# Performance work log

Measured on AMD Instinct MI355X. Metric: run time of the kernel, lower is better.

The kernel has to match this reference:

```python
import jax, jax.numpy as jnp
import numpy as np

B, H, W, DIM = 2, 128, 128, 256
NB, EXP, HEADS = 16, 8, 8
BS = DIM // NB          # AFNO block size = 16
DH = DIM // HEADS       # head dim = 32
EPS = 1e-5
LAM = 0.01              # softshrink threshold


def _ln(x, g, b):
    mu = jnp.mean(x, axis=-1, keepdims=True)
    var = jnp.mean((x - mu) ** 2, axis=-1, keepdims=True)
    return (x - mu) * jax.lax.rsqrt(var + EPS) * g + b


def _afno(x, w1, b1, w2, b2):
    # FourCastNet AFNO2D: block-diagonal complex MLP in Fourier space
    bias = x
    Bx, Hx, Wx, C = x.shape
    xf = jnp.fft.rfft2(x, axes=(1, 2), norm='ortho')          # [B,H,W//2+1,C] complex
    xf = xf.reshape(Bx, Hx, Wx // 2 + 1, NB, BS)
    xr, xi = jnp.real(xf), jnp.imag(xf)
    mm = lambda t, w: jnp.einsum('bhwni,nio->bhwno', t, w)
    o1r = jax.nn.relu(mm(xr, w1[0]) - mm(xi, w1[1]) + b1[0])
    o1i = jax.nn.relu(mm(xi, w1[0]) + mm(xr, w1[1]) + b1[1])
    o2r = mm(o1r, w2[0]) - mm(o1i, w2[1]) + b2[0]
    o2i = mm(o1i, w2[0]) + mm(o1r, w2[1]) + b2[1]
    shrink = lambda t: jnp.sign(t) * jnp.maximum(jnp.abs(t) - LAM, 0.0)
    xf = (shrink(o2r) + 1j * shrink(o2i)).reshape(Bx, Hx, Wx // 2 + 1, C)
    out = jnp.fft.irfft2(xf, s=(Hx, Wx), axes=(1, 2), norm='ortho')
    return out + bias


def _galerkin(h, wq, bq, wk, bk, wv, bv, lnk_g, lnk_b, lnv_g, lnv_b, wo, bo):
    # softmax-free linear attention: Q (LN(K)^T LN(V)) / N
    Bx, N, C = h.shape
    split = lambda t, w, b: (t @ w.T + b).reshape(Bx, N, HEADS, DH).transpose(0, 2, 1, 3)
    q = split(h, wq, bq)
    k = split(h, wk, bk)
    v = split(h, wv, bv)
    k = _ln(k, lnk_g[None, :, None, :], lnk_b[None, :, None, :])
    v = _ln(v, lnv_g[None, :, None, :], lnv_b[None, :, None, :])
    kv = jnp.einsum('bhnd,bhne->bhde', k, v) / N     # [B,h,dh,dh]
    out = jnp.einsum('bhnd,bhde->bhne', q, kv)       # [B,h,N,dh]
    out = out.transpose(0, 2, 1, 3).reshape(Bx, N, C)
    return out @ wo.T + bo


def _forward(x, afno_w1, afno_b1, afno_w2, afno_b2,
             wq, bq, wk, bk, wv, bv, lnk_g, lnk_b, lnv_g, lnv_b, wo, bo,
             w_up, b_up, w_down, b_down,
             n1_g, n1_b, n2_g, n2_b, n3_g, n3_b):
    Bx, Hx, Wx, C = x.shape
    # 1) AFNO spectral mixing block
    x = x + _afno(_ln(x, n1_g, n1_b), afno_w1, afno_b1, afno_w2, afno_b2)
    # 2) Galerkin linear attention block
    x = _ln(x, n2_g, n2_b)
    h = x.reshape(Bx, Hx * Wx, C)
    x = x + _galerkin(h, wq, bq, wk, bk, wv, bv,
                      lnk_g, lnk_b, lnv_g, lnv_b, wo, bo).reshape(Bx, Hx, Wx, C)
    # 3) pointwise-conv (1x1) FFN block; conv1x1 over BCHW == per-token linear in BHWC
    x = _ln(x, n3_g, n3_b)
    h = jax.nn.gelu(x @ w_up.T + b_up, approximate=False)
    x = x + h @ w_down.T + b_down
    return x


def setup_inputs() -> dict:
    key = jax.random.key(0)
    ks = jax.random.split(key, 24)
    r = lambda i, shape, s: jax.random.normal(ks[i], shape, dtype=jnp.float32) * s
    z = lambda shape: jnp.zeros(shape, dtype=jnp.float32)
    o = lambda shape: jnp.ones(shape, dtype=jnp.float32)
    return dict(
        x=r(0, (B, H, W, DIM), 1.0),
        afno_w1=r(1, (2, NB, BS, BS * EXP), 0.02),
        afno_b1=r(2, (2, NB, BS * EXP), 0.02),
        afno_w2=r(3, (2, NB, BS * EXP, BS), 0.02),
        afno_b2=r(4, (2, NB, BS), 0.02),
        wq=r(5, (DIM, DIM), 0.02), bq=z((DIM,)),
        wk=r(6, (DIM, DIM), 0.02), bk=z((DIM,)),
        wv=r(7, (DIM, DIM), 0.02), bv=z((DIM,)),
        lnk_g=o((HEADS, DH)), lnk_b=z((HEADS, DH)),
        lnv_g=o((HEADS, DH)), lnv_b=z((HEADS, DH)),
        wo=r(8, (DIM, DIM), 0.02), bo=z((DIM,)),
        w_up=r(9, (DIM * EXP, DIM), 0.02), b_up=z((DIM * EXP,)),
        w_down=r(10, (DIM, DIM * EXP), 0.02), b_down=z((DIM,)),
        n1_g=o((DIM,)), n1_b=z((DIM,)),
        n2_g=o((DIM,)), n2_b=z((DIM,)),
        n3_g=o((DIM,)), n3_b=z((DIM,)),
    )


def reference(x, afno_w1, afno_b1, afno_w2, afno_b2,
              wq, bq, wk, bk, wv, bv, lnk_g, lnk_b, lnv_g, lnv_b, wo, bo,
              w_up, b_up, w_down, b_down,
              n1_g, n1_b, n2_g, n2_b, n3_g, n3_b):
    return _forward(x, afno_w1, afno_b1, afno_w2, afno_b2,
                    wq, bq, wk, bk, wv, bv, lnk_g, lnk_b, lnv_g, lnv_b, wo, bo,
                    w_up, b_up, w_down, b_down,
                    n1_g, n1_b, n2_g, n2_b, n3_g, n3_b)
```

## Files before the change

### kernel.cpp

```cpp
#include <hip/hip_runtime.h>


typedef unsigned short u16;
typedef unsigned int u32;
typedef __attribute__((ext_vector_type(8))) short bf16x8;
typedef __attribute__((ext_vector_type(8))) unsigned short u16x8;
typedef __attribute__((ext_vector_type(4))) float f32x4;
#define DEV __device__ __forceinline__

constexpr int Cch = 256;
constexpr float EPSN = 1e-5f, LAM = 0.01f;
constexpr float TWO_PI = 6.283185307179586f;

DEV float b2f(u16 u) { return __uint_as_float(((u32)u) << 16); }
DEV u16 f2b(float f) {
  u32 x = __float_as_uint(f);
  return (u16)((x + 0x7FFFu + ((x >> 16) & 1u)) >> 16);
}

DEV void put2(u16* tw, int m, int idx, float v) {
  u16 hi = f2b(v);
  tw[m * 16384 + idx] = hi;
  tw[(m + 1) * 16384 + idx] = f2b(v - b2f(hi));
}

__global__ __launch_bounds__(128) void k_twid(u16* __restrict__ tw) {
  int p = blockIdx.x, q = threadIdx.x;
  int idx = p * 128 + q;
  float ang = TWO_PI * (float)((p * q) & 127) * (1.0f / 128.0f);
  float c = cosf(ang), s = sinf(ang);
  put2(tw, 0, idx, c * (1.0f / 128.0f));
  put2(tw, 2, idx, s * (1.0f / 128.0f));
  put2(tw, 4, idx, -s * (1.0f / 128.0f));
  put2(tw, 6, idx, c);
  put2(tw, 8, idx, s);
  put2(tw, 10, idx, -s);
  u16* wmh = tw + 196608;
  u16* wml = tw + 217088;
  for (int k = q; k < 160; k += 128) {
    float v = 0.0f;
    if (k < 65) {
      float sc = (k == 0 || k == 64) ? 1.0f : 2.0f;
      v = sc * cosf(TWO_PI * (float)((p * k) & 127) * (1.0f / 128.0f)) * (1.0f / 128.0f);
    } else if (k < 130) {
      int kk = k - 65;
      float sc = (kk == 0 || kk == 64) ? 1.0f : 2.0f;
      v = -sc * sinf(TWO_PI * (float)((p * kk) & 127) * (1.0f / 128.0f)) * (1.0f / 128.0f);
    }
    u16 hi = f2b(v);
    wmh[p * 160 + k] = hi;
    wml[p * 160 + k] = f2b(v - b2f(hi));
  }
}

__global__ __launch_bounds__(256) void k_wpack(const float* __restrict__ w1,
                                               const float* __restrict__ w2,
                                               u16* __restrict__ W1h, u16* __restrict__ W1l,
                                               u16* __restrict__ W2h, u16* __restrict__ W2l) {
  int idx = blockIdx.x * 256 + threadIdx.x;
  if (idx < 131072) {
    int n = idx >> 13, rem = idx & 8191;
    int out = rem >> 5, k = rem & 31;
    float v;
    if (out < 128)
      v = (k < 16) ? w1[((size_t)n * 16 + k) * 128 + out]
                   : -w1[((size_t)(16 + n) * 16 + (k - 16)) * 128 + out];
    else {
      int o = out - 128;
      v = (k < 16) ? w1[((size_t)(16 + n) * 16 + k) * 128 + o]
                   : w1[((size_t)n * 16 + (k - 16)) * 128 + o];
    }
    u16 hi = f2b(v);
    W1h[idx] = hi; W1l[idx] = f2b(v - b2f(hi));
  } else if (idx < 262144) {
    int id2 = idx - 131072;
    int n = id2 >> 13, rem = id2 & 8191;
    int out2 = rem >> 8, k = rem & 255;
    float v;
    if (out2 < 16)
      v = (k < 128) ? w2[((size_t)n * 128 + k) * 16 + out2]
                    : -w2[((size_t)(16 + n) * 128 + (k - 128)) * 16 + out2];
    else {
      int o = out2 - 16;
      v = (k < 128) ? w2[((size_t)(16 + n) * 128 + k) * 16 + o]
                    : w2[((size_t)n * 128 + (k - 128)) * 16 + o];
    }
    u16 hi = f2b(v);
    W2h[id2] = hi; W2l[id2] = f2b(v - b2f(hi));
  }
}

__global__ __launch_bounds__(256) void k_cvt2(const float* __restrict__ s0,
                                              const float* __restrict__ s1,
                                              u16* __restrict__ d0,
                                              u16* __restrict__ d1, int n) {
  int i = blockIdx.x * 256 + threadIdx.x;
  if (i < n) { d0[i] = f2b(s0[i]); d1[i] = f2b(s1[i]); }
}

template<int INF>
__global__ __launch_bounds__(256) void k_ln(const void* __restrict__ in,
                                            const float* __restrict__ g,
                                            const float* __restrict__ bta,
                                            u16* __restrict__ out) {
  int tid = threadIdx.x, lane = tid & 63;
  size_t token = (size_t)blockIdx.x * 4 + (tid >> 6);
  int c = lane * 4;
  float v[4];
  if (INF) {
    float4 f = *(const float4*)((const float*)in + token * Cch + c);
    v[0] = f.x; v[1] = f.y; v[2] = f.z; v[3] = f.w;
  } else {
    ushort4 u = *(const ushort4*)((const u16*)in + token * Cch + c);
    v[0] = b2f(u.x); v[1] = b2f(u.y); v[2] = b2f(u.z); v[3] = b2f(u.w);
  }
  float s = v[0] + v[1] + v[2] + v[3];
  #pragma unroll
  for (int m = 1; m < 64; m <<= 1) s += __shfl_xor(s, m);
  float mu = s * (1.0f / 256.0f);
  float q = 0.f;
  #pragma unroll
  for (int j = 0; j < 4; j++) { float d = v[j] - mu; q += d * d; }
  #pragma unroll
  for (int m = 1; m < 64; m <<= 1) q += __shfl_xor(q, m);
  float rs = rsqrtf(q * (1.0f / 256.0f) + EPSN);
  ushort4 o;
  o.x = f2b((v[0] - mu) * rs * g[c + 0] + bta[c + 0]);
  o.y = f2b((v[1] - mu) * rs * g[c + 1] + bta[c + 1]);
  o.z = f2b((v[2] - mu) * rs * g[c + 2] + bta[c + 2]);
  o.w = f2b((v[3] - mu) * rs * g[c + 3] + bta[c + 3]);
  *(ushort4*)(out + token * Cch + c) = o;
}

__global__ __launch_bounds__(256) void k_dftw_m(
    const u16* __restrict__ Yg,
    const u16* __restrict__ Chi_, const u16* __restrict__ Clo_,
    const u16* __restrict__ Shi_, const u16* __restrict__ Slo_,
    u16* __restrict__ Or, u16* __restrict__ Oi) {
  __shared__ u16 Bs[128][40];
  int tid = threadIdx.x;
  int bh = blockIdx.x;
  int c0 = blockIdx.y * 128;
  int lane = tid & 63, w = tid >> 6;
  int wm = w >> 1, wn = w & 1;
  int rl = lane & 15, kq = (lane >> 4) * 8, rq = lane >> 4;
  f32x4 accC[4][4] = {};
  f32x4 accS[4][4] = {};
  for (int k0 = 0; k0 < 128; k0 += 32) {
    __syncthreads();
    for (int idx = tid; idx < 1024; idx += 256) {
      int q = idx >> 5, c4 = (idx & 31) * 4;
      ushort4 v = *(const ushort4*)(Yg + ((size_t)bh * 128 + k0 + q) * 256 + c0 + c4);
      Bs[c4 + 0][q] = v.x; Bs[c4 + 1][q] = v.y;
      Bs[c4 + 2][q] = v.z; Bs[c4 + 3][q] = v.w;
    }
    __syncthreads();
    bf16x8 aCh[4], aCl[4], aSh[4], aSl[4], bf[4];
    #pragma unroll
    for (int i = 0; i < 4; i++) {
      int off = (wm * 64 + i * 16 + rl) * 128 + k0 + kq;
      aCh[i] = *(const bf16x8*)(Chi_ + off);
      aCl[i] = *(const bf16x8*)(Clo_ + off);
      aSh[i] = *(const bf16x8*)(Shi_ + off);
      aSl[i] = *(const bf16x8*)(Slo_ + off);
    }
    #pragma unroll
    for (int j = 0; j < 4; j++)
      bf[j] = *(const bf16x8*)&Bs[wn * 64 + j * 16 + rl][kq];
    #pragma unroll
    for (int i = 0; i < 4; i++)
      #pragma unroll
      for (int j = 0; j < 4; j++) {
        accC[i][j] = __builtin_amdgcn_mfma_f32_16x16x32_bf16(aCh[i], bf[j], accC[i][j], 0, 0, 0);
        accC[i][j] = __builtin_amdgcn_mfma_f32_16x16x32_bf16(aCl[i], bf[j], accC[i][j], 0, 0, 0);
        accS[i][j] = __builtin_amdgcn_mfma_f32_16x16x32_bf16(aSh[i], bf[j], accS[i][j], 0, 0, 0);
        accS[i][j] = __builtin_amdgcn_mfma_f32_16x16x32_bf16(aSl[i], bf[j], accS[i][j], 0, 0, 0);
      }
  }
  #pragma unroll
  for (int i = 0; i < 4; i++)
    #pragma unroll
    for (int j = 0; j < 4; j++)
      #pragma unroll
      for (int r = 0; r < 4; r++) {
        int p = wm * 64 + i * 16 + rq * 4 + r;
        if (p < 65) {
          int c = c0 + wn * 64 + j * 16 + rl;
          size_t g = ((size_t)bh * 65 + p) * 256 + c;
          Or[g] = f2b(accC[i][j][r]);
          Oi[g] = f2b(accS[i][j][r]);
        }
      }
}

__global__ __launch_bounds__(256) void k_dfth_m(
    const u16* __restrict__ Br_g, const u16* __restrict__ Bi_g,
    const u16* __restrict__ Chi, const u16* __restrict__ Clo,
    const u16* __restrict__ SRhi, const u16* __restrict__ SRlo,
    const u16* __restrict__ SIhi, const u16* __restrict__ SIlo,
    u16* __restrict__ Or, u16* __restrict__ Oi) {
  __shared__ u16 B1s[128][40], B2s[128][40];
  int tid = threadIdx.x;
  int bk = blockIdx.x;
  int b = bk / 65, kw = bk % 65;
  int c0 = (blockIdx.y & 1) * 128;
  int outI = blockIdx.y >> 1;
  const u16* B1g = outI ? Bi_g : Br_g;
  const u16* B2g = outI ? Br_g : Bi_g;
  const u16* Shi = outI ? SIhi : SRhi;
  const u16* Slo = outI ? SIlo : SRlo;
  u16* outp = outI ? Oi : Or;
  int lane = tid & 63, w = tid >> 6;
  int wm = w >> 1, wn = w & 1;
  int rl = lane & 15, kq = (lane >> 4) * 8, rq = lane >> 4;
  f32x4 acc[4][4] = {};
  for (int k0 = 0; k0 < 128; k0 += 32) {
    __syncthreads();
    for (int idx = tid; idx < 1024; idx += 256) {
      int q = idx >> 5, c4 = (idx & 31) * 4;
      size_t g = (((size_t)b * 128 + k0 + q) * 65 + kw) * 256 + c0 + c4;
      ushort4 v1 = *(const ushort4*)(B1g + g);
      ushort4 v2 = *(const ushort4*)(B2g + g);
      B1s[c4 + 0][q] = v1.x; B1s[c4 + 1][q] = v1.y;
      B1s[c4 + 2][q] = v1.z; B1s[c4 + 3][q] = v1.w;
      B2s[c4 + 0][q] = v2.x; B2s[c4 + 1][q] = v2.y;
      B2s[c4 + 2][q] = v2.z; B2s[c4 + 3][q] = v2.w;
    }
    __syncthreads();
    bf16x8 aCh[4], aCl[4], aSh[4], aSl[4], b1[4], b2[4];
    #pragma unroll
    for (int i = 0; i < 4; i++) {
      int off = (wm * 64 + i * 16 + rl) * 128 + k0 + kq;
      aCh[i] = *(const bf16x8*)(Chi + off);
      aCl[i] = *(const bf16x8*)(Clo + off);
      aSh[i] = *(const bf16x8*)(Shi + off);
      aSl[i] = *(const bf16x8*)(Slo + off);
    }
    #pragma unroll
    for (int j = 0; j < 4; j++) {
      b1[j] = *(const bf16x8*)&B1s[wn * 64 + j * 16 + rl][kq];
      b2[j] = *(const bf16x8*)&B2s[wn * 64 + j * 16 + rl][kq];
    }
    #pragma unroll
    for (int i = 0; i < 4; i++)
      #pragma unroll
      for (int j = 0; j < 4; j++) {
        acc[i][j] = __builtin_amdgcn_mfma_f32_16x16x32_bf16(aCh[i], b1[j], acc[i][j], 0, 0, 0);
        acc[i][j] = __builtin_amdgcn_mfma_f32_16x16x32_bf16(aCl[i], b1[j], acc[i][j], 0, 0, 0);
        acc[i][j] = __builtin_amdgcn_mfma_f32_16x16x32_bf16(aSh[i], b2[j], acc[i][j], 0, 0, 0);
        acc[i][j] = __builtin_amdgcn_mfma_f32_16x16x32_bf16(aSl[i], b2[j], acc[i][j], 0, 0, 0);
      }
  }
  #pragma unroll
  for (int i = 0; i < 4; i++)
    #pragma unroll
    for (int j = 0; j < 4; j++)
      #pragma unroll
      for (int r = 0; r < 4; r++) {
        int p = wm * 64 + i * 16 + rq * 4 + r;
        int c = c0 + wn * 64 + j * 16 + rl;
        outp[(((size_t)b * 128 + p) * 65 + kw) * 256 + c] = f2b(acc[i][j][r]);
      }
}

__global__ __launch_bounds__(256) void k_irfft_m(
    const u16* __restrict__ Ur, const u16* __restrict__ Ui,
    const u16* __restrict__ Whi, const u16* __restrict__ Wlo,
    const float* __restrict__ x_in, const u16* __restrict__ lnout,
    u16* __restrict__ X1) {
  __shared__ u16 Bs[128][40];
  int tid = threadIdx.x;
  int bh = blockIdx.x;
  int c0 = blockIdx.y * 128;
  int lane = tid & 63, w = tid >> 6;
  int wm = w >> 1, wn = w & 1;
  int rl = lane & 15, kq = (lane >> 4) * 8, rq = lane >> 4;
  f32x4 acc[4][4] = {};
  for (int k0 = 0; k0 < 160; k0 += 32) {
    __syncthreads();
    for (int idx = tid; idx < 1024; idx += 256) {
      int q = idx >> 5, c4 = (idx & 31) * 4;
      int grow = k0 + q;
      ushort4 v;
      if (grow < 65)
        v = *(const ushort4*)(Ur + ((size_t)bh * 65 + grow) * 256 + c0 + c4);
      else if (grow < 130)
        v = *(const ushort4*)(Ui + ((size_t)bh * 65 + grow - 65) * 256 + c0 + c4);
      else
        v = make_ushort4(0, 0, 0, 0);
      Bs[c4 + 0][q] = v.x; Bs[c4 + 1][q] = v.y;
      Bs[c4 + 2][q] = v.z; Bs[c4 + 3][q] = v.w;
    }
    __syncthreads();
    bf16x8 ah[4], al[4], bf[4];
    #pragma unroll
    for (int i = 0; i < 4; i++) {
      int off = (wm * 64 + i * 16 + rl) * 160 + k0 + kq;
      ah[i] = *(const bf16x8*)(Whi + off);
      al[i] = *(const bf16x8*)(Wlo + off);
    }
    #pragma unroll
    for (int j = 0; j < 4; j++)
      bf[j] = *(const bf16x8*)&Bs[wn * 64 + j * 16 + rl][kq];
    #pragma unroll
    for (int i = 0; i < 4; i++)
      #pragma unroll
      for (int j = 0; j < 4; j++) {
        acc[i][j] = __builtin_amdgcn_mfma_f32_16x16x32_bf16(ah[i], bf[j], acc[i][j], 0, 0, 0);
        acc[i][j] = __builtin_amdgcn_mfma_f32_16x16x32_bf16(al[i], bf[j], acc[i][j], 0, 0, 0);
      }
  }
  #pragma unroll
  for (int i = 0; i < 4; i++)
    #pragma unroll
    for (int j = 0; j < 4; j++)
      #pragma unroll
      for (int r = 0; r < 4; r++) {
        int p = wm * 64 + i * 16 + rq * 4 + r;
        int c = c0 + wn * 64 + j * 16 + rl;
        size_t g = ((size_t)bh * 128 + p) * 256 + c;
        X1[g] = f2b(x_in[g] + b2f(lnout[g]) + acc[i][j][r]);
      }
}

__global__ __launch_bounds__(256) void k_afno_mfma(
    const u16* __restrict__ Zr, const u16* __restrict__ Zi,
    const u16* __restrict__ W1h, const u16* __restrict__ W1l,
    const u16* __restrict__ W2h, const u16* __restrict__ W2l,
    const float* __restrict__ b1, const float* __restrict__ b2,
    u16* __restrict__ Or, u16* __restrict__ Oi) {
  __shared__ u16 o1buf[4][64][74];
  int tid = threadIdx.x;
  int lane = tid & 63, w = tid >> 6;
  int n = blockIdx.x * 4 + w;
  int p0 = blockIdx.y * 64;
  int rl = lane & 15, rq = lane >> 4, kq = rq * 8;
  bf16x8 bfr[4];
  #pragma unroll
  for (int j = 0; j < 4; j++) {
    int p = p0 + j * 16 + rl;
    const u16* src = (kq < 16) ? (Zr + (size_t)p * 256 + n * 16 + kq)
                               : (Zi + (size_t)p * 256 + n * 16 + kq - 16);
    bfr[j] = *(const bf16x8*)src;
  }
  f32x4 acc2[2][4] = {};
  for (int c = 0; c < 4; c++) {
    f32x4 a1[4][4] = {};
    #pragma unroll
    for (int i = 0; i < 4; i++) {
      int out = c * 64 + i * 16 + rl;
      bf16x8 ah = *(const bf16x8*)(W1h + ((size_t)n * 256 + out) * 32 + kq);
      bf16x8 al = *(const bf16x8*)(W1l + ((size_t)n * 256 + out) * 32 + kq);
      #pragma unroll
      for (int j = 0; j < 4; j++) {
        a1[i][j] = __builtin_amdgcn_mfma_f32_16x16x32_bf16(ah, bfr[j], a1[i][j], 0, 0, 0);
        a1[i][j] = __builtin_amdgcn_mfma_f32_16x16x32_bf16(al, bfr[j], a1[i][j], 0, 0, 0);
      }
    }
    #pragma unroll
    for (int i = 0; i < 4; i++) {
      float bv[4];
      #pragma unroll
      for (int r = 0; r < 4; r++) {
        int out = c * 64 + i * 16 + rq * 4 + r;
        bv[r] = (out < 128) ? b1[n * 128 + out] : b1[2048 + n * 128 + out - 128];
      }
      #pragma unroll
      for (int j = 0; j < 4; j++) {
        int pos = j * 16 + rl;
        ushort4 pk;
        u16* pp = &pk.x;
        #pragma unroll
        for (int r = 0; r < 4; r++)
          pp[r] = f2b(fmaxf(a1[i][j][r] + bv[r], 0.0f));
        *(ushort4*)&o1buf[w][pos][(i * 16 + rq * 4) ^ ((pos & 7) << 3)] = pk;
      }
    }
    #pragma unroll
    for (int ks = 0; ks < 2; ks++) {
      int kg = c * 64 + ks * 32 + kq;
      #pragma unroll
      for (int i2 = 0; i2 < 2; i2++) {
        int out2 = i2 * 16 + rl;
        bf16x8 ah = *(const bf16x8*)(W2h + ((size_t)n * 32 + out2) * 256 + kg);
        bf16x8 al = *(const bf16x8*)(W2l + ((size_t)n * 32 + out2) * 256 + kg);
        #pragma unroll
        for (int j = 0; j < 4; j++) {
          int pos = j * 16 + rl;
          bf16x8 bb = *(const bf16x8*)&o1buf[w][pos][(ks * 32 + kq) ^ ((pos & 7) << 3)];
          acc2[i2][j] = __builtin_amdgcn_mfma_f32_16x16x32_bf16(ah, bb, acc2[i2][j], 0, 0, 0);
          acc2[i2][j] = __builtin_amdgcn_mfma_f32_16x16x32_bf16(al, bb, acc2[i2][j], 0, 0, 0);
        }
      }
    }
  }
  #pragma unroll
  for (int i2 = 0; i2 < 2; i2++)
    #pragma unroll
    for (int r = 0; r < 4; r++) {
      int out2 = i2 * 16 + rq * 4 + r;
      float bv = (out2 < 16) ? b2[n * 16 + out2] : b2[256 + n * 16 + out2 - 16];
      int ch = (out2 < 16) ? out2 : out2 - 16;
      #pragma unroll
      for (int j = 0; j < 4; j++) {
        float v = acc2[i2][j][r] + bv;
        v = copysignf(fmaxf(fabsf(v) - LAM, 0.0f), v);
        size_t g = (size_t)(p0 + j * 16 + rl) * 256 + n * 16 + ch;
        if (out2 < 16) Or[g] = f2b(v);
        else Oi[g] = f2b(v);
      }
    }
}

template<int ACT, int RT, int OUTF>
__global__ __launch_bounds__(256) void k_mgemm(const u16* __restrict__ Ap,
                                               const u16* __restrict__ Bp,
                                               const float* __restrict__ bias,
                                               const u16* __restrict__ resid,
                                               void* __restrict__ Cp,
                                               int M, int N, int K) {
  __shared__ u16 As[128][40];
  __shared__ u16 Bs[128][40];
  int tid = threadIdx.x;
  int lane = tid & 63, w = tid >> 6;
  int wm = w >> 1, wn = w & 1;
  int m0 = blockIdx.x * 128, n0 = blockIdx.y * 128;
  int srow = tid >> 1, sseg = tid & 1;
  const u16* ag = Ap + (size_t)(m0 + srow) * K + sseg * 16;
  const u16* bg = Bp + (size_t)(n0 + srow) * K + sseg * 16;
  int rl = lane & 15, kq = (lane >> 4) * 8;
  f32x4 acc[4][4] = {};
  for (int k0 = 0; k0 < K; k0 += 32) {
    __syncthreads();
    *(u16x8*)&As[srow][sseg * 16]     = *(const u16x8*)(ag + k0);
    *(u16x8*)&As[srow][sseg * 16 + 8] = *(const u16x8*)(ag + k0 + 8);
    *(u16x8*)&Bs[srow][sseg * 16]     = *(const u16x8*)(bg + k0);
    *(u16x8*)&Bs[srow][sseg * 16 + 8] = *(const u16x8*)(bg + k0 + 8);
    __syncthreads();
    bf16x8 af[4], bf[4];
    #pragma unroll
    for (int i = 0; i < 4; i++) {
      af[i] = *(const bf16x8*)&As[wm * 64 + i * 16 + rl][kq];
      bf[i] = *(const bf16x8*)&Bs[wn * 64 + i * 16 + rl][kq];
    }
    #pragma unroll
    for (int i = 0; i < 4; i++)
      #pragma unroll
      for (int j = 0; j < 4; j++)
        acc[i][j] = __builtin_amdgcn_mfma_f32_16x16x32_bf16(af[i], bf[j], acc[i][j], 0, 0, 0);
  }
  int rq = lane >> 4;
  #pragma unroll
  for (int i = 0; i < 4; i++) {
    #pragma unroll
    for (int j = 0; j < 4; j++) {
      #pragma unroll
      for (int r = 0; r < 4; r++) {
        int m = m0 + wm * 64 + i * 16 + rq * 4 + r;
        int n = n0 + wn * 64 + j * 16 + rl;
        float v = acc[i][j][r] + bias[n];
        if (ACT) v = 0.5f * v * (1.0f + erff(v * 0.70710678118654752f));
        if (RT) v += b2f(resid[(size_t)m * N + n]);
        if (OUTF) ((float*)Cp)[(size_t)m * N + n] = v;
        else ((u16*)Cp)[(size_t)m * N + n] = f2b(v);
      }
    }
  }
}

__global__ __launch_bounds__(256) void k_mgemm_qkv(
    const u16* __restrict__ Ap,
    const u16* __restrict__ Wk, const u16* __restrict__ Wv, const u16* __restrict__ Wq,
    const float* __restrict__ bk, const float* __restrict__ bv, const float* __restrict__ bq,
    u16* __restrict__ Ko, u16* __restrict__ Vo, u16* __restrict__ Qo) {
  __shared__ u16 As[128][40];
  __shared__ u16 Bs[128][40];
  int sel = blockIdx.y >> 1;
  const u16* Bp = (sel == 0) ? Wk : (sel == 1) ? Wv : Wq;
  const float* bias = (sel == 0) ? bk : (sel == 1) ? bv : bq;
  u16* Cp = (sel == 0) ? Ko : (sel == 1) ? Vo : Qo;
  int tid = threadIdx.x;
  int lane = tid & 63, w = tid >> 6;
  int wm = w >> 1, wn = w & 1;
  int m0 = blockIdx.x * 128, n0 = (blockIdx.y & 1) * 128;
  int srow = tid >> 1, sseg = tid & 1;
  const u16* ag = Ap + (size_t)(m0 + srow) * 256 + sseg * 16;
  const u16* bg = Bp + (size_t)(n0 + srow) * 256 + sseg * 16;
  int rl = lane & 15, kq = (lane >> 4) * 8;
  f32x4 acc[4][4] = {};
  for (int k0 = 0; k0 < 256; k0 += 32) {
    __syncthreads();
    *(u16x8*)&As[srow][sseg * 16]     = *(const u16x8*)(ag + k0);
    *(u16x8*)&As[srow][sseg * 16 + 8] = *(const u16x8*)(ag + k0 + 8);
    *(u16x8*)&Bs[srow][sseg * 16]     = *(const u16x8*)(bg + k0);
    *(u16x8*)&Bs[srow][sseg * 16 + 8] = *(const u16x8*)(bg + k0 + 8);
    __syncthreads();
    bf16x8 af[4], bf[4];
    #pragma unroll
    for (int i = 0; i < 4; i++) {
      af[i] = *(const bf16x8*)&As[wm * 64 + i * 16 + rl][kq];
      bf[i] = *(const bf16x8*)&Bs[wn * 64 + i * 16 + rl][kq];
    }
    #pragma unroll
    for (int i = 0; i < 4; i++)
      #pragma unroll
      for (int j = 0; j < 4; j++)
        acc[i][j] = __builtin_amdgcn_mfma_f32_16x16x32_bf16(af[i], bf[j], acc[i][j], 0, 0, 0);
  }
  int rq = lane >> 4;
  #pragma unroll
  for (int i = 0; i < 4; i++)
    #pragma unroll
    for (int j = 0; j < 4; j++)
      #pragma unroll
      for (int r = 0; r < 4; r++) {
        int m = m0 + wm * 64 + i * 16 + rq * 4 + r;
        int n = n0 + wn * 64 + j * 16 + rl;
        Cp[(size_t)m * 256 + n] = f2b(acc[i][j][r] + bias[n]);
      }
}

__global__ __launch_bounds__(256) void k_mgemm_d(const u16* __restrict__ Ap,
                                                 const u16* __restrict__ Bp,
                                                 const float* __restrict__ bias,
                                                 const u16* __restrict__ resid,
                                                 float* __restrict__ Cp,
                                                 int M, int N, int K) {
  __shared__ u16 As[64][40];
  __shared__ u16 Bs[64][40];
  int tid = threadIdx.x;
  int lane = tid & 63, w = tid >> 6;
  int wm = w >> 1, wn = w & 1;
  int m0 = blockIdx.x * 64, n0 = blockIdx.y * 64;
  int srow = tid >> 2, sseg = tid & 3;
  const u16* ag = Ap + (size_t)(m0 + srow) * K + sseg * 8;
  const u16* bg = Bp + (size_t)(n0 + srow) * K + sseg * 8;
  int rl = lane & 15, kq = (lane >> 4) * 8;
  f32x4 acc[2][2] = {};
  for (int k0 = 0; k0 < K; k0 += 32) {
    __syncthreads();
    *(u16x8*)&As[srow][sseg * 8] = *(const u16x8*)(ag + k0);
    *(u16x8*)&Bs[srow][sseg * 8] = *(const u16x8*)(bg + k0);
    __syncthreads();
    bf16x8 af[2], bf[2];
    #pragma unroll
    for (int i = 0; i < 2; i++) {
      af[i] = *(const bf16x8*)&As[wm * 32 + i * 16 + rl][kq];
      bf[i] = *(const bf16x8*)&Bs[wn * 32 + i * 16 + rl][kq];
    }
    #pragma unroll
    for (int i = 0; i < 2; i++)
      #pragma unroll
      for (int j = 0; j < 2; j++)
        acc[i][j] = __builtin_amdgcn_mfma_f32_16x16x32_bf16(af[i], bf[j], acc[i][j], 0, 0, 0);
  }
  int rq = lane >> 4;
  #pragma unroll
  for (int i = 0; i < 2; i++)
    #pragma unroll
    for (int j = 0; j < 2; j++)
      #pragma unroll
      for (int r = 0; r < 4; r++) {
        int m = m0 + wm * 32 + i * 16 + rq * 4 + r;
        int n = n0 + wn * 32 + j * 16 + rl;
        float v = acc[i][j][r] + bias[n] + b2f(resid[(size_t)m * N + n]);
        Cp[(size_t)m * N + n] = v;
      }
}

__global__ __launch_bounds__(256) void k_lnhead2(u16* __restrict__ K,
                                                 u16* __restrict__ V,
                                                 const float* __restrict__ kg,
                                                 const float* __restrict__ kb,
                                                 const float* __restrict__ vg,
                                                 const float* __restrict__ vb) {
  int tid = threadIdx.x, lane = tid & 63;
  u16* X = blockIdx.y ? V : K;
  const float* g = blockIdx.y ? vg : kg;
  const float* bta = blockIdx.y ? vb : kb;
  size_t token = (size_t)blockIdx.x * 4 + (tid >> 6);
  int c = lane * 4;
  ushort4 u = *(const ushort4*)(X + token * Cch + c);
  float v[4] = {b2f(u.x), b2f(u.y), b2f(u.z), b2f(u.w)};
  float s = v[0] + v[1] + v[2] + v[3];
  s += __shfl_xor(s, 1); s += __shfl_xor(s, 2); s += __shfl_xor(s, 4);
  float mu = s * (1.0f / 32.0f);
  float q = 0.f;
  #pragma unroll
  for (int j = 0; j < 4; j++) { float d = v[j] - mu; q += d * d; }
  q += __shfl_xor(q, 1); q += __shfl_xor(q, 2); q += __shfl_xor(q, 4);
  float rs = rsqrtf(q * (1.0f / 32.0f) + EPSN);
  ushort4 o;
  o.x = f2b((v[0] - mu) * rs * g[c + 0] + bta[c + 0]);
  o.y = f2b((v[1] - mu) * rs * g[c + 1] + bta[c + 1]);
  o.z = f2b((v[2] - mu) * rs * g[c + 2] + bta[c + 2]);
  o.w = f2b((v[3] - mu) * rs * g[c + 3] + bta[c + 3]);
  *(ushort4*)(X + token * Cch + c) = o;
}

__global__ __launch_bounds__(256) void k_kv_partial(const u16* __restrict__ Kb,
                                                    const u16* __restrict__ Vb,
                                                    float* __restrict__ part) {
  __shared__ float kl[64][33], vl[64][33];
  int tid = threadIdx.x;
  int bh = blockIdx.x;
  int b = bh >> 3, h = bh & 7;
  int n0 = blockIdx.y * 1024;
  int d = tid >> 3, eg = tid & 7;
  float acc[4] = {0.f, 0.f, 0.f, 0.f};
  for (int sub = 0; sub < 16; sub++) {
    __syncthreads();
    for (int idx = tid; idx < 64 * 32; idx += 256) {
      int nn = idx >> 5, c = idx & 31;
      size_t o = ((size_t)(b * 16384 + n0 + sub * 64 + nn)) * Cch + h * 32 + c;
      kl[nn][c] = b2f(Kb[o]); vl[nn][c] = b2f(Vb[o]);
    }
    __syncthreads();
    #pragma unroll 4
    for (int nn = 0; nn < 64; nn++) {
      float kd = kl[nn][d];
      #pragma unroll
      for (int j = 0; j < 4; j++) acc[j] += kd * vl[nn][eg * 4 + j];
    }
  }
  size_t base = ((size_t)bh * 16 + blockIdx.y) * 1024 + d * 32 + eg * 4;
  #pragma unroll
  for (int j = 0; j < 4; j++) part[base + j] = acc[j];
}

__global__ __launch_bounds__(1024) void k_kv_reduce(const float* __restrict__ part,
                                                    u16* __restrict__ kvTh,
                                                    u16* __restrict__ kvTl) {
  int bh = blockIdx.x, o = threadIdx.x;
  float s = 0.f;
  #pragma unroll
  for (int p = 0; p < 16; p++) s += part[((size_t)bh * 16 + p) * 1024 + o];
  s *= (1.0f / 16384.0f);
  int d = o >> 5, e = o & 31;
  u16 hi = f2b(s);
  kvTh[(size_t)bh * 1024 + e * 32 + d] = hi;
  kvTl[(size_t)bh * 1024 + e * 32 + d] = f2b(s - b2f(hi));
}

__global__ __launch_bounds__(256) void k_attn_m(const u16* __restrict__ Q,
                                                const u16* __restrict__ kvTh,
                                                const u16* __restrict__ kvTl,
                                                u16* __restrict__ ATT) {
  int tid = threadIdx.x;
  int lane = tid & 63, w = tid >> 6;
  int h = blockIdx.y;
  int t0 = blockIdx.x * 64 + w * 16;
  int b = t0 >> 14;
  int rl = lane & 15, rq = lane >> 4, kq = rq * 8;
  bf16x8 a = *(const bf16x8*)(Q + (size_t)(t0 + rl) * 256 + h * 32 + kq);
  const u16* kh = kvTh + (size_t)(b * 8 + h) * 1024;
  const u16* kl = kvTl + (size_t)(b * 8 + h) * 1024;
  f32x4 acc[2] = {};
  #pragma unroll
  for (int j = 0; j < 2; j++) {
    bf16x8 bh_ = *(const bf16x8*)(kh + (j * 16 + rl) * 32 + kq);
    bf16x8 bl_ = *(const bf16x8*)(kl + (j * 16 + rl) * 32 + kq);
    acc[j] = __builtin_amdgcn_mfma_f32_16x16x32_bf16(a, bh_, acc[j], 0, 0, 0);
    acc[j] = __builtin_amdgcn_mfma_f32_16x16x32_bf16(a, bl_, acc[j], 0, 0, 0);
  }
  #pragma unroll
  for (int j = 0; j < 2; j++)
    #pragma unroll
    for (int r = 0; r < 4; r++)
      ATT[(size_t)(t0 + rq * 4 + r) * 256 + h * 32 + j * 16 + rl] = f2b(acc[j][r]);
}

extern "C" void kernel_launch(void* const* d_in, const int* in_sizes, int n_in,
                              void* d_out, int out_size, void* d_ws, size_t ws_size,
                              hipStream_t stream) {
  (void)in_sizes; (void)n_in; (void)out_size; (void)ws_size;
  const float* x    = (const float*)d_in[0];
  const float* w1   = (const float*)d_in[1];
  const float* b1   = (const float*)d_in[2];
  const float* w2   = (const float*)d_in[3];
  const float* b2   = (const float*)d_in[4];
  const float* wq   = (const float*)d_in[5];
  const float* bq   = (const float*)d_in[6];
  const float* wk   = (const float*)d_in[7];
  const float* bk   = (const float*)d_in[8];
  const float* wv   = (const float*)d_in[9];
  const float* bv   = (const float*)d_in[10];
  const float* lnkg = (const float*)d_in[11];
  const float* lnkb = (const float*)d_in[12];
  const float* lnvg = (const float*)d_in[13];
  const float* lnvb = (const float*)d_in[14];
  const float* wo   = (const float*)d_in[15];
  const float* bo   = (const float*)d_in[16];
  const float* wup  = (const float*)d_in[17];
  const float* bup  = (const float*)d_in[18];
  const float* wdn  = (const float*)d_in[19];
  const float* bdn  = (const float*)d_in[20];
  const float* n1g  = (const float*)d_in[21];
  const float* n1b  = (const float*)d_in[22];
  const float* n2g  = (const float*)d_in[23];
  const float* n2b  = (const float*)d_in[24];
  const float* n3g  = (const float*)d_in[25];
  const float* n3b  = (const float*)d_in[26];

  char* ws = (char*)d_ws;
  u16* A    = (u16*)(ws + 0);
  u16* S1r  = (u16*)(ws + 16777216);
  u16* S1i  = (u16*)(ws + 25296896);
  u16* S2r  = (u16*)(ws + 33816576);
  u16* S2i  = (u16*)(ws + 42336256);
  u16* X1   = (u16*)(ws + 16777216);
  u16* Vb   = (u16*)(ws + 16777216);
  u16* X2   = (u16*)(ws + 16777216);
  u16* Kb   = (u16*)(ws + 33816576);
  u16* ATT  = (u16*)(ws + 33816576);
  u16* UP   = (u16*)(ws + 33816576);
  u16* wq_b = (u16*)(ws + 33554432);
  u16* wk_b = (u16*)(ws + 33685504);
  u16* wv_b = (u16*)(ws + 50593792);
  u16* wo_b = (u16*)(ws + 50724864);
  u16* wup_b = (u16*)(ws + 16777216);
  u16* wdn_b = (u16*)(ws + 17825792);
  u16* TW   = (u16*)(ws + 50855936);
  float* KVp = (float*)(ws + 50855936);
  u16* kvTh = (u16*)(ws + 51904512);
  u16* kvTl = (u16*)(ws + 51937280);
  float* outp = (float*)d_out;
  u16* Qb  = (u16*)d_out;
  u16* W1h = (u16*)d_out;
  u16* W1l = W1h + 131072;
  u16* W2h = W1h + 262144;
  u16* W2l = W1h + 393216;

  u16 *Cf_h = TW + 0 * 16384, *Cf_l = TW + 1 * 16384;
  u16 *Sf_h = TW + 2 * 16384, *Sf_l = TW + 3 * 16384;
  u16 *Snf_h = TW + 4 * 16384, *Snf_l = TW + 5 * 16384;
  u16 *Cu_h = TW + 6 * 16384, *Cu_l = TW + 7 * 16384;
  u16 *Su_h = TW + 8 * 16384, *Su_l = TW + 9 * 16384;
  u16 *Snu_h = TW + 10 * 16384, *Snu_l = TW + 11 * 16384;
  u16 *Wm_h = TW + 196608, *Wm_l = TW + 217088;

  k_twid<<<128, 128, 0, stream>>>(TW);
  k_wpack<<<1024, 256, 0, stream>>>(w1, w2, W1h, W1l, W2h, W2l);

  k_ln<1><<<8192, 256, 0, stream>>>((const void*)x, n1g, n1b, A);
  k_dftw_m<<<dim3(256, 2), 256, 0, stream>>>(A, Cu_h, Cu_l, Snu_h, Snu_l, S1r, S1i);
  k_dfth_m<<<dim3(130, 4), 256, 0, stream>>>(S1r, S1i, Cf_h, Cf_l, Sf_h, Sf_l, Snf_h, Snf_l, S2r, S2i);
  k_afno_mfma<<<dim3(4, 260), 256, 0, stream>>>(S2r, S2i, W1h, W1l, W2h, W2l, b1, b2, S1r, S1i);
  k_dfth_m<<<dim3(130, 4), 256, 0, stream>>>(S1r, S1i, Cu_h, Cu_l, Snu_h, Snu_l, Su_h, Su_l, S2r, S2i);
  k_irfft_m<<<dim3(256, 2), 256, 0, stream>>>(S2r, S2i, Wm_h, Wm_l, x, A, X1);

  k_cvt2<<<256, 256, 0, stream>>>(wq, wk, wq_b, wk_b, 65536);
  k_cvt2<<<256, 256, 0, stream>>>(wv, wo, wv_b, wo_b, 65536);

  k_ln<0><<<8192, 256, 0, stream>>>((const void*)X1, n2g, n2b, A);
  k_mgemm_qkv<<<dim3(256, 6), 256, 0, stream>>>(A, wk_b, wv_b, wq_b, bk, bv, bq, Kb, Vb, Qb);
  k_lnhead2<<<dim3(8192, 2), 256, 0, stream>>>(Kb, Vb, lnkg, lnkb, lnvg, lnvb);
  k_kv_partial<<<dim3(16, 16), 256, 0, stream>>>(Kb, Vb, KVp);
  k_kv_reduce<<<16, 1024, 0, stream>>>(KVp, kvTh, kvTl);
  k_attn_m<<<dim3(512, 8), 256, 0, stream>>>(Qb, kvTh, kvTl, ATT);
  k_mgemm<0, 1, 0><<<dim3(256, 2), 256, 0, stream>>>(ATT, wo_b, bo, A, (void*)X2, 32768, 256, 256);

  k_ln<0><<<8192, 256, 0, stream>>>((const void*)X2, n3g, n3b, A);
  k_cvt2<<<2048, 256, 0, stream>>>(wup, wdn, wup_b, wdn_b, 524288);
  for (int c = 0; c < 8; c++) {
    const u16* Ac = A + (size_t)c * 4096 * 256;
    k_mgemm<1, 0, 0><<<dim3(32, 16), 256, 0, stream>>>(Ac, wup_b, bup, nullptr, (void*)UP, 4096, 2048, 256);
    k_mgemm_d<<<dim3(64, 4), 256, 0, stream>>>(UP, wdn_b, bdn, Ac, outp + (size_t)c * 4096 * 256, 4096, 256, 2048);
  }
}
```

Baseline: 743.0 us.

## Software-pipeline FFN chunks, fuse head LayerNorm into QKV GEMM, merge init kernels

The FFN now runs in 16 chunks of 2048 rows. Each launch computes the up-projection of chunk c and the down-projection of chunk c-1 together, using double-buffered UP storage, so the two GEMMs overlap within one grid and fill the GPU better. The per-head K/V LayerNorm moves into the QKV GEMM epilogue, using shuffle reductions across the 32-wide head slice, which removes the separate k_lnhead2 pass over K and V. The twiddle and weight-pack kernels, and the two weight-conversion kernels, are each merged into a single launch to cut launch count. The cost is more launches in the FFN loop, smaller per-launch tiles, and a more complex epilogue in the QKV GEMM.

```diff
diff --git a/kernel.cpp b/kernel.cpp
--- a/kernel.cpp
+++ b/kernel.cpp
@@ -24,70 +24,86 @@
   tw[(m + 1) * 16384 + idx] = f2b(v - b2f(hi));
 }
 
-__global__ __launch_bounds__(128) void k_twid(u16* __restrict__ tw) {
-  int p = blockIdx.x, q = threadIdx.x;
-  int idx = p * 128 + q;
-  float ang = TWO_PI * (float)((p * q) & 127) * (1.0f / 128.0f);
-  float c = cosf(ang), s = sinf(ang);
-  put2(tw, 0, idx, c * (1.0f / 128.0f));
-  put2(tw, 2, idx, s * (1.0f / 128.0f));
-  put2(tw, 4, idx, -s * (1.0f / 128.0f));
-  put2(tw, 6, idx, c);
-  put2(tw, 8, idx, s);
-  put2(tw, 10, idx, -s);
-  u16* wmh = tw + 196608;
-  u16* wml = tw + 217088;
-  for (int k = q; k < 160; k += 128) {
-    float v = 0.0f;
-    if (k < 65) {
-      float sc = (k == 0 || k == 64) ? 1.0f : 2.0f;
-      v = sc * cosf(TWO_PI * (float)((p * k) & 127) * (1.0f / 128.0f)) * (1.0f / 128.0f);
-    } else if (k < 130) {
-      int kk = k - 65;
-      float sc = (kk == 0 || kk == 64) ? 1.0f : 2.0f;
-      v = -sc * sinf(TWO_PI * (float)((p * kk) & 127) * (1.0f / 128.0f)) * (1.0f / 128.0f);
-    }
-    u16 hi = f2b(v);
-    wmh[p * 160 + k] = hi;
-    wml[p * 160 + k] = f2b(v - b2f(hi));
-  }
-}
-
-__global__ __launch_bounds__(256) void k_wpack(const float* __restrict__ w1,
-                                               const float* __restrict__ w2,
-                                               u16* __restrict__ W1h, u16* __restrict__ W1l,
-                                               u16* __restrict__ W2h, u16* __restrict__ W2l) {
-  int idx = blockIdx.x * 256 + threadIdx.x;
-  if (idx < 131072) {
-    int n = idx >> 13, rem = idx & 8191;
-    int out = rem >> 5, k = rem & 31;
-    float v;
-    if (out < 128)
-      v = (k < 16) ? w1[((size_t)n * 16 + k) * 128 + out]
-                   : -w1[((size_t)(16 + n) * 16 + (k - 16)) * 128 + out];
-    else {
-      int o = out - 128;
-      v = (k < 16) ? w1[((size_t)(16 + n) * 16 + k) * 128 + o]
-                   : w1[((size_t)n * 16 + (k - 16)) * 128 + o];
-    }
-    u16 hi = f2b(v);
-    W1h[idx] = hi; W1l[idx] = f2b(v - b2f(hi));
-  } else if (idx < 262144) {
-    int id2 = idx - 131072;
-    int n = id2 >> 13, rem = id2 & 8191;
-    int out2 = rem >> 8, k = rem & 255;
-    float v;
-    if (out2 < 16)
-      v = (k < 128) ? w2[((size_t)n * 128 + k) * 16 + out2]
-                    : -w2[((size_t)(16 + n) * 128 + (k - 128)) * 16 + out2];
-    else {
-      int o = out2 - 16;
-      v = (k < 128) ? w2[((size_t)(16 + n) * 128 + k) * 16 + o]
-                    : w2[((size_t)n * 128 + (k - 128)) * 16 + o];
-    }
-    u16 hi = f2b(v);
-    W2h[id2] = hi; W2l[id2] = f2b(v - b2f(hi));
-  }
+__global__ __launch_bounds__(256) void k_init(const float* __restrict__ w1,
+                                              const float* __restrict__ w2,
+                                              u16* __restrict__ W1h, u16* __restrict__ W1l,
+                                              u16* __restrict__ W2h, u16* __restrict__ W2l,
+                                              u16* __restrict__ tw) {
+  int bid = blockIdx.x;
+  if (bid < 1024) {
+    int idx = bid * 256 + threadIdx.x;
+    if (idx < 131072) {
+      int n = idx >> 13, rem = idx & 8191;
+      int out = rem >> 5, k = rem & 31;
+      float v;
+      if (out < 128)
+        v = (k < 16) ? w1[((size_t)n * 16 + k) * 128 + out]
+                     : -w1[((size_t)(16 + n) * 16 + (k - 16)) * 128 + out];
+      else {
+        int o = out - 128;
+        v = (k < 16) ? w1[((size_t)(16 + n) * 16 + k) * 128 + o]
+                     : w1[((size_t)n * 16 + (k - 16)) * 128 + o];
+      }
+      u16 hi = f2b(v);
+      W1h[idx] = hi; W1l[idx] = f2b(v - b2f(hi));
+    } else if (idx < 262144) {
+      int id2 = idx - 131072;
+      int n = id2 >> 13, rem = id2 & 8191;
+      int out2 = rem >> 8, k = rem & 255;
+      float v;
+      if (out2 < 16)
+        v = (k < 128) ? w2[((size_t)n * 128 + k) * 16 + out2]
+                      : -w2[((size_t)(16 + n) * 128 + (k - 128)) * 16 + out2];
+      else {
+        int o = out2 - 16;
+        v = (k < 128) ? w2[((size_t)(16 + n) * 128 + k) * 16 + o]
+                      : w2[((size_t)n * 128 + (k - 128)) * 16 + o];
+      }
+      u16 hi = f2b(v);
+      W2h[id2] = hi; W2l[id2] = f2b(v - b2f(hi));
+    }
+  } else {
+    int q = threadIdx.x;
+    if (q < 128) {
+      int p = bid - 1024;
+      int idx = p * 128 + q;
+      float ang = TWO_PI * (float)((p * q) & 127) * (1.0f / 128.0f);
+      float c = cosf(ang), s = sinf(ang);
+      put2(tw, 0, idx, c * (1.0f / 128.0f));
+      put2(tw, 2, idx, s * (1.0f / 128.0f));
+      put2(tw, 4, idx, -s * (1.0f / 128.0f));
+      put2(tw, 6, idx, c);
+      put2(tw, 8, idx, s);
+      put2(tw, 10, idx, -s);
+      u16* wmh = tw + 196608;
+      u16* wml = tw + 217088;
+      for (int k = q; k < 160; k += 128) {
+        float v = 0.0f;
+        if (k < 65) {
+          float sc = (k == 0 || k == 64) ? 1.0f : 2.0f;
+          v = sc * cosf(TWO_PI * (float)((p * k) & 127) * (1.0f / 128.0f)) * (1.0f / 128.0f);
+        } else if (k < 130) {
+          int kk = k - 65;
+          float sc = (kk == 0 || kk == 64) ? 1.0f : 2.0f;
+          v = -sc * sinf(TWO_PI * (float)((p * kk) & 127) * (1.0f / 128.0f)) * (1.0f / 128.0f);
+        }
+        u16 hi = f2b(v);
+        wmh[p * 160 + k] = hi;
+        wml[p * 160 + k] = f2b(v - b2f(hi));
+      }
+    }
+  }
+}
+
+__global__ __launch_bounds__(256) void k_cvt4(const float* __restrict__ s0,
+                                              const float* __restrict__ s1,
+                                              const float* __restrict__ s2,
+                                              const float* __restrict__ s3,
+                                              u16* __restrict__ d0, u16* __restrict__ d1,
+                                              u16* __restrict__ d2, u16* __restrict__ d3,
+                                              int n) {
+  int i = blockIdx.x * 256 + threadIdx.x;
+  if (i < n) { d0[i] = f2b(s0[i]); d1[i] = f2b(s1[i]); d2[i] = f2b(s2[i]); d3[i] = f2b(s3[i]); }
 }
 
 __global__ __launch_bounds__(256) void k_cvt2(const float* __restrict__ s0,
@@ -472,6 +488,8 @@
     const u16* __restrict__ Ap,
     const u16* __restrict__ Wk, const u16* __restrict__ Wv, const u16* __restrict__ Wq,
     const float* __restrict__ bk, const float* __restrict__ bv, const float* __restrict__ bq,
+    const float* __restrict__ lnkg, const float* __restrict__ lnkb,
+    const float* __restrict__ lnvg, const float* __restrict__ lnvb,
     u16* __restrict__ Ko, u16* __restrict__ Vo, u16* __restrict__ Qo) {
   __shared__ u16 As[128][40];
   __shared__ u16 Bs[128][40];
@@ -508,94 +526,132 @@
         acc[i][j] = __builtin_amdgcn_mfma_f32_16x16x32_bf16(af[i], bf[j], acc[i][j], 0, 0, 0);
   }
   int rq = lane >> 4;
-  #pragma unroll
-  for (int i = 0; i < 4; i++)
-    #pragma unroll
-    for (int j = 0; j < 4; j++)
+  if (sel == 2) {
+    #pragma unroll
+    for (int i = 0; i < 4; i++)
+      #pragma unroll
+      for (int j = 0; j < 4; j++)
+        #pragma unroll
+        for (int r = 0; r < 4; r++) {
+          int m = m0 + wm * 64 + i * 16 + rq * 4 + r;
+          int n = n0 + wn * 64 + j * 16 + rl;
+          Cp[(size_t)m * 256 + n] = f2b(acc[i][j][r] + bias[n]);
+        }
+  } else {
+    const float* g = sel ? lnvg : lnkg;
+    const float* bt = sel ? lnvb : lnkb;
+    #pragma unroll
+    for (int i = 0; i < 4; i++)
       #pragma unroll
       for (int r = 0; r < 4; r++) {
         int m = m0 + wm * 64 + i * 16 + rq * 4 + r;
-        int n = n0 + wn * 64 + j * 16 + rl;
-        Cp[(size_t)m * 256 + n] = f2b(acc[i][j][r] + bias[n]);
-      }
-}
-
-__global__ __launch_bounds__(256) void k_mgemm_d(const u16* __restrict__ Ap,
-                                                 const u16* __restrict__ Bp,
-                                                 const float* __restrict__ bias,
-                                                 const u16* __restrict__ resid,
-                                                 float* __restrict__ Cp,
-                                                 int M, int N, int K) {
-  __shared__ u16 As[64][40];
-  __shared__ u16 Bs[64][40];
+        #pragma unroll
+        for (int hb = 0; hb < 2; hb++) {
+          int hbase = n0 + wn * 64 + hb * 32;
+          float v0 = acc[i][hb * 2 + 0][r] + bias[hbase + rl];
+          float v1 = acc[i][hb * 2 + 1][r] + bias[hbase + 16 + rl];
+          float s = v0 + v1;
+          s += __shfl_xor(s, 1); s += __shfl_xor(s, 2);
+          s += __shfl_xor(s, 4); s += __shfl_xor(s, 8);
+          float mu = s * (1.0f / 32.0f);
+          float q = (v0 - mu) * (v0 - mu) + (v1 - mu) * (v1 - mu);
+          q += __shfl_xor(q, 1); q += __shfl_xor(q, 2);
+          q += __shfl_xor(q, 4); q += __shfl_xor(q, 8);
+          float rs = rsqrtf(q * (1.0f / 32.0f) + EPSN);
+          float o0 = (v0 - mu) * rs * g[hbase + rl] + bt[hbase + rl];
+          float o1 = (v1 - mu) * rs * g[hbase + 16 + rl] + bt[hbase + 16 + rl];
+          Cp[(size_t)m * 256 + hbase + rl] = f2b(o0);
+          Cp[(size_t)m * 256 + hbase + 16 + rl] = f2b(o1);
+        }
+      }
+  }
+}
+
+__global__ __launch_bounds__(256) void k_ffn_step(
+    const u16* __restrict__ Aup, const u16* __restrict__ Wup,
+    const float* __restrict__ bup, u16* __restrict__ UPw,
+    const u16* __restrict__ UPr, const u16* __restrict__ Wdn,
+    const float* __restrict__ bdn, const u16* __restrict__ Adown,
+    float* __restrict__ outc, int nDown) {
+  __shared__ u16 As[128][40];
+  __shared__ u16 Bs[128][40];
+  int bid = blockIdx.x;
   int tid = threadIdx.x;
   int lane = tid & 63, w = tid >> 6;
   int wm = w >> 1, wn = w & 1;
-  int m0 = blockIdx.x * 64, n0 = blockIdx.y * 64;
-  int srow = tid >> 2, sseg = tid & 3;
-  const u16* ag = Ap + (size_t)(m0 + srow) * K + sseg * 8;
-  const u16* bg = Bp + (size_t)(n0 + srow) * K + sseg * 8;
-  int rl = lane & 15, kq = (lane >> 4) * 8;
-  f32x4 acc[2][2] = {};
-  for (int k0 = 0; k0 < K; k0 += 32) {
-    __syncthreads();
-    *(u16x8*)&As[srow][sseg * 8] = *(const u16x8*)(ag + k0);
-    *(u16x8*)&Bs[srow][sseg * 8] = *(const u16x8*)(bg + k0);
-    __syncthreads();
-    bf16x8 af[2], bf[2];
-    #pragma unroll
-    for (int i = 0; i < 2; i++) {
-      af[i] = *(const bf16x8*)&As[wm * 32 + i * 16 + rl][kq];
-      bf[i] = *(const bf16x8*)&Bs[wn * 32 + i * 16 + rl][kq];
+  int rl = lane & 15, kq = (lane >> 4) * 8, rq = lane >> 4;
+  if (bid < nDown) {
+    int m0 = (bid & 31) * 64, n0 = (bid >> 5) * 64;
+    int srow = tid >> 2, sseg = tid & 3;
+    const u16* ag = UPr + (size_t)(m0 + srow) * 2048 + sseg * 8;
+    const u16* bg = Wdn + (size_t)(n0 + srow) * 2048 + sseg * 8;
+    f32x4 acc[2][2] = {};
+    for (int k0 = 0; k0 < 2048; k0 += 32) {
+      __syncthreads();
+      *(u16x8*)&As[srow][sseg * 8] = *(const u16x8*)(ag + k0);
+      *(u16x8*)&Bs[srow][sseg * 8] = *(const u16x8*)(bg + k0);
+      __syncthreads();
+      bf16x8 af[2], bf[2];
+      #pragma unroll
+      for (int i = 0; i < 2; i++) {
+        af[i] = *(const bf16x8*)&As[wm * 32 + i * 16 + rl][kq];
+        bf[i] = *(const bf16x8*)&Bs[wn * 32 + i * 16 + rl][kq];
+      }
+      #pragma unroll
+      for (int i = 0; i < 2; i++)
+        #pragma unroll
+        for (int j = 0; j < 2; j++)
+          acc[i][j] = __builtin_amdgcn_mfma_f32_16x16x32_bf16(af[i], bf[j], acc[i][j], 0, 0, 0);
     }
     #pragma unroll
     for (int i = 0; i < 2; i++)
       #pragma unroll
       for (int j = 0; j < 2; j++)
-        acc[i][j] = __builtin_amdgcn_mfma_f32_16x16x32_bf16(af[i], bf[j], acc[i][j], 0, 0, 0);
-  }
-  int rq = lane >> 4;
-  #pragma unroll
-  for (int i = 0; i < 2; i++)
-    #pragma unroll
-    for (int j = 0; j < 2; j++)
-      #pragma unroll
-      for (int r = 0; r < 4; r++) {
-        int m = m0 + wm * 32 + i * 16 + rq * 4 + r;
-        int n = n0 + wn * 32 + j * 16 + rl;
-        float v = acc[i][j][r] + bias[n] + b2f(resid[(size_t)m * N + n]);
-        Cp[(size_t)m * N + n] = v;
-      }
-}
-
-__global__ __launch_bounds__(256) void k_lnhead2(u16* __restrict__ K,
-                                                 u16* __restrict__ V,
-                                                 const float* __restrict__ kg,
-                                                 const float* __restrict__ kb,
-                                                 const float* __restrict__ vg,
-                                                 const float* __restrict__ vb) {
-  int tid = threadIdx.x, lane = tid & 63;
-  u16* X = blockIdx.y ? V : K;
-  const float* g = blockIdx.y ? vg : kg;
-  const float* bta = blockIdx.y ? vb : kb;
-  size_t token = (size_t)blockIdx.x * 4 + (tid >> 6);
-  int c = lane * 4;
-  ushort4 u = *(const ushort4*)(X + token * Cch + c);
-  float v[4] = {b2f(u.x), b2f(u.y), b2f(u.z), b2f(u.w)};
-  float s = v[0] + v[1] + v[2] + v[3];
-  s += __shfl_xor(s, 1); s += __shfl_xor(s, 2); s += __shfl_xor(s, 4);
-  float mu = s * (1.0f / 32.0f);
-  float q = 0.f;
-  #pragma unroll
-  for (int j = 0; j < 4; j++) { float d = v[j] - mu; q += d * d; }
-  q += __shfl_xor(q, 1); q += __shfl_xor(q, 2); q += __shfl_xor(q, 4);
-  float rs = rsqrtf(q * (1.0f / 32.0f) + EPSN);
-  ushort4 o;
-  o.x = f2b((v[0] - mu) * rs * g[c + 0] + bta[c + 0]);
-  o.y = f2b((v[1] - mu) * rs * g[c + 1] + bta[c + 1]);
-  o.z = f2b((v[2] - mu) * rs * g[c + 2] + bta[c + 2]);
-  o.w = f2b((v[3] - mu) * rs * g[c + 3] + bta[c + 3]);
-  *(ushort4*)(X + token * Cch + c) = o;
+        #pragma unroll
+        for (int r = 0; r < 4; r++) {
+          int m = m0 + wm * 32 + i * 16 + rq * 4 + r;
+          int n = n0 + wn * 32 + j * 16 + rl;
+          outc[(size_t)m * 256 + n] = acc[i][j][r] + bdn[n] + b2f(Adown[(size_t)m * 256 + n]);
+        }
+  } else {
+    int u = bid - nDown;
+    int m0 = (u & 15) * 128, n0 = (u >> 4) * 128;
+    int srow = tid >> 1, sseg = tid & 1;
+    const u16* ag = Aup + (size_t)(m0 + srow) * 256 + sseg * 16;
+    const u16* bg = Wup + (size_t)(n0 + srow) * 256 + sseg * 16;
+    f32x4 acc[4][4] = {};
+    for (int k0 = 0; k0 < 256; k0 += 32) {
+      __syncthreads();
+      *(u16x8*)&As[srow][sseg * 16]     = *(const u16x8*)(ag + k0);
+      *(u16x8*)&As[srow][sseg * 16 + 8] = *(const u16x8*)(ag + k0 + 8);
+      *(u16x8*)&Bs[srow][sseg * 16]     = *(const u16x8*)(bg + k0);
+      *(u16x8*)&Bs[srow][sseg * 16 + 8] = *(const u16x8*)(bg + k0 + 8);
+      __syncthreads();
+      bf16x8 af[4], bf[4];
+      #pragma unroll
+      for (int i = 0; i < 4; i++) {
+        af[i] = *(const bf16x8*)&As[wm * 64 + i * 16 + rl][kq];
+        bf[i] = *(const bf16x8*)&Bs[wn * 64 + i * 16 + rl][kq];
+      }
+      #pragma unroll
+      for (int i = 0; i < 4; i++)
+        #pragma unroll
+        for (int j = 0; j < 4; j++)
+          acc[i][j] = __builtin_amdgcn_mfma_f32_16x16x32_bf16(af[i], bf[j], acc[i][j], 0, 0, 0);
+    }
+    #pragma unroll
+    for (int i = 0; i < 4; i++)
+      #pragma unroll
+      for (int j = 0; j < 4; j++)
+        #pragma unroll
+        for (int r = 0; r < 4; r++) {
+          int m = m0 + wm * 64 + i * 16 + rq * 4 + r;
+          int n = n0 + wn * 64 + j * 16 + rl;
+          float v = acc[i][j][r] + bup[n];
+          v = 0.5f * v * (1.0f + erff(v * 0.70710678118654752f));
+          UPw[(size_t)m * 2048 + n] = f2b(v);
+        }
+  }
 }
 
 __global__ __launch_bounds__(256) void k_kv_partial(const u16* __restrict__ Kb,
@@ -713,7 +769,8 @@
   u16* X2   = (u16*)(ws + 16777216);
   u16* Kb   = (u16*)(ws + 33816576);
   u16* ATT  = (u16*)(ws + 33816576);
-  u16* UP   = (u16*)(ws + 33816576);
+  u16* UP_A = (u16*)(ws + 33816576);
+  u16* UP_B = (u16*)(ws + 42205184);
   u16* wq_b = (u16*)(ws + 33554432);
   u16* wk_b = (u16*)(ws + 33685504);
   u16* wv_b = (u16*)(ws + 50593792);
@@ -739,8 +796,7 @@
   u16 *Snu_h = TW + 10 * 16384, *Snu_l = TW + 11 * 16384;
   u16 *Wm_h = TW + 196608, *Wm_l = TW + 217088;
 
-  k_twid<<<128, 128, 0, stream>>>(TW);
-  k_wpack<<<1024, 256, 0, stream>>>(w1, w2, W1h, W1l, W2h, W2l);
+  k_init<<<1152, 256, 0, stream>>>(w1, w2, W1h, W1l, W2h, W2l, TW);
 
   k_ln<1><<<8192, 256, 0, stream>>>((const void*)x, n1g, n1b, A);
   k_dftw_m<<<dim3(256, 2), 256, 0, stream>>>(A, Cu_h, Cu_l, Snu_h, Snu_l, S1r, S1i);
@@ -749,12 +805,11 @@
   k_dfth_m<<<dim3(130, 4), 256, 0, stream>>>(S1r, S1i, Cu_h, Cu_l, Snu_h, Snu_l, Su_h, Su_l, S2r, S2i);
   k_irfft_m<<<dim3(256, 2), 256, 0, stream>>>(S2r, S2i, Wm_h, Wm_l, x, A, X1);
 
-  k_cvt2<<<256, 256, 0, stream>>>(wq, wk, wq_b, wk_b, 65536);
-  k_cvt2<<<256, 256, 0, stream>>>(wv, wo, wv_b, wo_b, 65536);
+  k_cvt4<<<256, 256, 0, stream>>>(wq, wk, wv, wo, wq_b, wk_b, wv_b, wo_b, 65536);
 
   k_ln<0><<<8192, 256, 0, stream>>>((const void*)X1, n2g, n2b, A);
-  k_mgemm_qkv<<<dim3(256, 6), 256, 0, stream>>>(A, wk_b, wv_b, wq_b, bk, bv, bq, Kb, Vb, Qb);
-  k_lnhead2<<<dim3(8192, 2), 256, 0, stream>>>(Kb, Vb, lnkg, lnkb, lnvg, lnvb);
+  k_mgemm_qkv<<<dim3(256, 6), 256, 0, stream>>>(A, wk_b, wv_b, wq_b, bk, bv, bq,
+                                                lnkg, lnkb, lnvg, lnvb, Kb, Vb, Qb);
   k_kv_partial<<<dim3(16, 16), 256, 0, stream>>>(Kb, Vb, KVp);
   k_kv_reduce<<<16, 1024, 0, stream>>>(KVp, kvTh, kvTl);
   k_attn_m<<<dim3(512, 8), 256, 0, stream>>>(Qb, kvTh, kvTl, ATT);
@@ -762,9 +817,17 @@
 
   k_ln<0><<<8192, 256, 0, stream>>>((const void*)X2, n3g, n3b, A);
   k_cvt2<<<2048, 256, 0, stream>>>(wup, wdn, wup_b, wdn_b, 524288);
-  for (int c = 0; c < 8; c++) {
-    const u16* Ac = A + (size_t)c * 4096 * 256;
-    k_mgemm<1, 0, 0><<<dim3(32, 16), 256, 0, stream>>>(Ac, wup_b, bup, nullptr, (void*)UP, 4096, 2048, 256);
-    k_mgemm_d<<<dim3(64, 4), 256, 0, stream>>>(UP, wdn_b, bdn, Ac, outp + (size_t)c * 4096 * 256, 4096, 256, 2048);
-  }
-}
+  u16* UPbuf[2] = {UP_A, UP_B};
+  k_ffn_step<<<256, 256, 0, stream>>>(A, wup_b, bup, UPbuf[0],
+                                      UP_A, wdn_b, bdn, A, outp, 0);
+  for (int c = 1; c < 16; c++) {
+    const u16* Aup = A + (size_t)c * 2048 * 256;
+    const u16* Adn = A + (size_t)(c - 1) * 2048 * 256;
+    k_ffn_step<<<384, 256, 0, stream>>>(Aup, wup_b, bup, UPbuf[c & 1],
+                                        UPbuf[(c - 1) & 1], wdn_b, bdn, Adn,
+                                        outp + (size_t)(c - 1) * 2048 * 256, 128);
+  }
+  k_ffn_step<<<128, 256, 0, stream>>>(A, wup_b, bup, UP_A,
+                                      UPbuf[1], wdn_b, bdn, A + (size_t)15 * 2048 * 256,
+                                      outp + (size_t)15 * 2048 * 256, 128);
+}
```

Result: slower. 793.7 us (+6.8%).
